# Optimization experiments

Hardware: AMD Instinct MI355X
Metric: run time of the kernel (lower is better)

The kernel has to match this reference:

```python
import jax, jax.numpy as jnp
import numpy as np

HIDDEN = 64
EPS = 0.001


def _gru_cell(x, h, w_ih, w_hh, b_ih, b_hh):
    # PyTorch GRUCell math. w_ih: [3H, D], w_hh: [3H, H], gates ordered (r, z, n).
    gi = x @ w_ih.T + b_ih  # [B, 3H]
    gh = h @ w_hh.T + b_hh  # [B, 3H]
    i_r, i_z, i_n = jnp.split(gi, 3, axis=-1)
    h_r, h_z, h_n = jnp.split(gh, 3, axis=-1)
    r = jax.nn.sigmoid(i_r + h_r)
    z = jax.nn.sigmoid(i_z + h_z)
    n = jnp.tanh(i_n + r * h_n)
    return (1.0 - z) * n + z * h


def setup_inputs() -> dict:
    key = jax.random.key(0)
    ks = jax.random.split(key, 12)
    B, T, state_dim, action_dim = 2048, 512, 64, 8
    H = HIDDEN
    k_in = 1.0 / np.sqrt(H)  # PyTorch GRUCell init bound
    u = lambda k, shp: jax.random.uniform(k, shp, jnp.float32, -k_in, k_in)
    return {
        "state": jax.random.normal(ks[0], (B, T, state_dim), jnp.float32),
        "w_ih1": u(ks[1], (3 * H, state_dim)),
        "w_hh1": u(ks[2], (3 * H, H)),
        "b_ih1": u(ks[3], (3 * H,)),
        "b_hh1": u(ks[4], (3 * H,)),
        "w_ih2": u(ks[5], (3 * H, H)),
        "w_hh2": u(ks[6], (3 * H, H)),
        "b_ih2": u(ks[7], (3 * H,)),
        "b_hh2": u(ks[8], (3 * H,)),
        "fc_w": jax.random.uniform(ks[9], (action_dim, H), jnp.float32, -EPS, EPS),
        "fc_b": u(ks[10], (action_dim,)),
    }


def reference(state, w_ih1, w_hh1, b_ih1, b_hh1, w_ih2, w_hh2, b_ih2, b_hh2, fc_w, fc_b):
    B = state.shape[0]
    h0 = jnp.zeros((B, HIDDEN), state.dtype)

    def step(carry, x_t):
        s1, s2 = carry
        s1 = _gru_cell(x_t, s1, w_ih1, w_hh1, b_ih1, b_hh1)
        s2 = _gru_cell(s1, s2, w_ih2, w_hh2, b_ih2, b_hh2)
        return (s1, s2), None

    xs = jnp.swapaxes(state, 0, 1)  # [T, B, state_dim]
    (_, s2), _ = jax.lax.scan(step, (h0, h0), xs)
    return s2 @ fc_w.T + fc_b  # [B, action_dim]
```

## Files before the change

### kernel.cpp

```cpp
#include <hip/hip_runtime.h>

#define T_STEPS 512
#define HID 64
#define SPB 8
#define NT 512

typedef _Float16 f16x8 __attribute__((ext_vector_type(8)));
typedef float f32x4 __attribute__((ext_vector_type(4)));

#define MFMA(a, b, c) __builtin_amdgcn_mfma_f32_16x16x32_f16(a, b, c, 0, 0, 0)

#define LOG2E 1.44269504088896340736f

__device__ __forceinline__ unsigned pkh(float a, float b) {
    unsigned short ua = __builtin_bit_cast(unsigned short, (_Float16)a);
    unsigned short ub = __builtin_bit_cast(unsigned short, (_Float16)b);
    return (unsigned)ua | ((unsigned)ub << 16);
}
__device__ __forceinline__ float dpp_ror8(float x) {
    int i = __builtin_bit_cast(int, x);
    int r = __builtin_amdgcn_mov_dpp(i, 0x128, 0xF, 0xF, true);
    return __builtin_bit_cast(float, r);
}
__device__ __forceinline__ char* swz(const void* base, int s, int kbyte) {
    int off = s * 128 + kbyte;
    off ^= (s & 7) << 4;
    return (char*)base + off;
}
__device__ __forceinline__ f16x8 g8rowS(const float* __restrict__ p, float s) {
    f16x8 r;
#pragma unroll
    for (int j = 0; j < 8; ++j) r[j] = (_Float16)(p[j] * s);
    return r;
}

#define BAR() do { asm volatile("s_waitcnt lgkmcnt(0)" ::: "memory"); \
                   __builtin_amdgcn_s_barrier();                      \
                   asm volatile("" ::: "memory"); } while (0)

__global__ __launch_bounds__(NT, 1)
void gru2_h16(const float* __restrict__ state,
              const float* __restrict__ w_ih1, const float* __restrict__ w_hh1,
              const float* __restrict__ b_ih1, const float* __restrict__ b_hh1,
              const float* __restrict__ w_ih2, const float* __restrict__ w_hh2,
              const float* __restrict__ b_ih2, const float* __restrict__ b_hh2,
              const float* __restrict__ fc_w,  const float* __restrict__ fc_b,
              float* __restrict__ out)
{
    __shared__ __align__(16) unsigned short xb[2][16][64];
    __shared__ __align__(16) unsigned short h1b[2][16][64];
    __shared__ __align__(16) unsigned short h2b[2][16][64];

    const int tid  = threadIdx.x;
    const int wv8  = tid >> 6;
    const bool isA = wv8 < 4;
    const int w    = wv8 & 3;
    const int lane = tid & 63;
    const int i16  = lane & 15;
    const int g    = lane >> 4;
    const int g8   = g * 8;
    const int b0   = blockIdx.x * SPB;
    const bool realc = (i16 < 8);

    const float* Wp = isA ? w_ih1 : w_ih2;
    const float* Wq = isA ? w_hh1 : w_hh2;
    const float* Bi = isA ? b_ih1 : b_ih2;
    const float* Bh = isA ? b_hh1 : b_hh2;

    const int rA = (16 * w + i16) * HID;
    const int zA = rA + 64 * HID;
    const int nA = rA + 128 * HID;
    f16x8 ar[4], az[4], ani[2], anh[2];
    ar[0]  = g8rowS(Wp + rA + g8, -LOG2E);  ar[1]  = g8rowS(Wp + rA + 32 + g8, -LOG2E);
    ar[2]  = g8rowS(Wq + rA + g8, -LOG2E);  ar[3]  = g8rowS(Wq + rA + 32 + g8, -LOG2E);
    az[0]  = g8rowS(Wp + zA + g8, -LOG2E);  az[1]  = g8rowS(Wp + zA + 32 + g8, -LOG2E);
    az[2]  = g8rowS(Wq + zA + g8, -LOG2E);  az[3]  = g8rowS(Wq + zA + 32 + g8, -LOG2E);
    ani[0] = g8rowS(Wp + nA + g8, 2.0f * LOG2E);
    ani[1] = g8rowS(Wp + nA + 32 + g8, 2.0f * LOG2E);
    anh[0] = g8rowS(Wq + nA + g8, 2.0f * LOG2E);
    anh[1] = g8rowS(Wq + nA + 32 + g8, 2.0f * LOG2E);

    f32x4 bR4, bZ4, bNi4, bNh4;
#pragma unroll
    for (int q = 0; q < 4; ++q) {
        const int r0 = 16 * w + 4 * g + q;
        bR4[q]  = -LOG2E * (Bi[r0] + Bh[r0]);
        bZ4[q]  = -LOG2E * (Bi[64 + r0] + Bh[64 + r0]);
        bNi4[q] = 2.0f * LOG2E * Bi[128 + r0];
        bNh4[q] = 2.0f * LOG2E * Bh[128 + r0];
    }

    char* rp[2][2]; char* rq[2][2]; char* wd[2]; char* sa[2];
    const int scol = i16 & 7;
    const int qb4  = realc ? 0 : 4;
#pragma unroll
    for (int c = 0; c < 2; ++c) {
        const void* Pb = isA ? (const void*)xb[c]      : (const void*)h1b[c ^ 1];
        const void* Qb = isA ? (const void*)h1b[c ^ 1] : (const void*)h2b[c];
        void* Db       = isA ? (void*)h1b[c]           : (void*)h2b[c ^ 1];
        rp[c][0] = swz(Pb, i16, 16 * g);
        rp[c][1] = swz(Pb, i16, 64 + 16 * g);
        rq[c][0] = swz(Qb, i16, 16 * g);
        rq[c][1] = swz(Qb, i16, 64 + 16 * g);
        wd[c]    = swz(Db, scol, 32 * w + 8 * g + qb4);
        sa[c]    = swz(xb[c ^ 1], (tid >> 5) & 7, (tid & 31) * 4);
    }

    for (int k = tid; k < 2 * 16 * 64; k += NT) {
        ((unsigned short*)xb)[k]  = 0;
        ((unsigned short*)h1b)[k] = 0;
        ((unsigned short*)h2b)[k] = 0;
    }
    __syncthreads();

    const int ss = (tid >> 5) & 7;
    const int sk = (tid & 31) * 2;
    const float* xgp = state + (size_t)(b0 + ss) * T_STEPS * HID + sk;
    float2 PF = make_float2(0.0f, 0.0f);
    if (tid < 256) {
        float2 v0 = *(const float2*)xgp;
        *(unsigned*)swz(xb[0], ss, sk * 2) = pkh(v0.x, v0.y);
        PF = *(const float2*)(xgp + HID);
    }
    const float* xnext = xgp + 2 * HID;
    __syncthreads();

    float hr0 = 0.0f, hr1 = 0.0f;
    f16x8 p0 = {}, p1 = {}, q0 = {}, q1 = {};

#define ITER(TT, CUR)                                                            \
  {                                                                              \
    const bool active = isA ? ((TT) < T_STEPS) : ((TT) >= 1);                    \
    if (active) {                                                                \
      if (realc) {       \
        p0 = *(const f16x8*)rp[CUR][0];                                          \
        p1 = *(const f16x8*)rp[CUR][1];                                          \
        q0 = *(const f16x8*)rq[CUR][0];                                          \
        q1 = *(const f16x8*)rq[CUR][1];                                          \
      }                                                                          \
      __builtin_amdgcn_s_setprio(1);                                             \
      f32x4 aR  = MFMA(ar[0], p0, bR4);                                          \
      f32x4 aZ  = MFMA(az[0], p0, bZ4);                                          \
      f32x4 aNi = MFMA(ani[0], p0, bNi4);                                        \
      f32x4 aNh = MFMA(anh[0], q0, bNh4);                                        \
      aR  = MFMA(ar[1], p1, aR);   aR  = MFMA(ar[2], q0, aR);                    \
      aR  = MFMA(ar[3], q1, aR);                                                 \
      aZ  = MFMA(az[1], p1, aZ);   aZ  = MFMA(az[2], q0, aZ);                    \
      aZ  = MFMA(az[3], q1, aZ);                                                 \
      aNi = MFMA(ani[1], p1, aNi);                                               \
      aNh = MFMA(anh[1], q1, aNh);                                               \
      __builtin_amdgcn_s_setprio(0);                                             \
        \
      float vR0  = realc ? aR[0]  : dpp_ror8(aR[2]);                             \
      float vR1  = realc ? aR[1]  : dpp_ror8(aR[3]);                             \
      float vZ0  = realc ? aZ[0]  : dpp_ror8(aZ[2]);                             \
      float vZ1  = realc ? aZ[1]  : dpp_ror8(aZ[3]);                             \
      float vNi0 = realc ? aNi[0] : dpp_ror8(aNi[2]);                            \
      float vNi1 = realc ? aNi[1] : dpp_ror8(aNi[3]);                            \
      float vNh0 = realc ? aNh[0] : dpp_ror8(aNh[2]);                            \
      float vNh1 = realc ? aNh[1] : dpp_ror8(aNh[3]);                            \
      {                                                                          \
        float rg0 = __builtin_amdgcn_rcpf(1.0f + __builtin_amdgcn_exp2f(vR0));   \
        float zg0 = __builtin_amdgcn_rcpf(1.0f + __builtin_amdgcn_exp2f(vZ0));   \
        float e20 = __builtin_amdgcn_exp2f(fmaf(rg0, vNh0, vNi0));               \
        float ng0 = fmaf(-2.0f, __builtin_amdgcn_rcpf(1.0f + e20), 1.0f);        \
        hr0 = fmaf(zg0, hr0 - ng0, ng0);                                         \
        float rg1 = __builtin_amdgcn_rcpf(1.0f + __builtin_amdgcn_exp2f(vR1));   \
        float zg1 = __builtin_amdgcn_rcpf(1.0f + __builtin_amdgcn_exp2f(vZ1));   \
        float e21 = __builtin_amdgcn_exp2f(fmaf(rg1, vNh1, vNi1));               \
        float ng1 = fmaf(-2.0f, __builtin_amdgcn_rcpf(1.0f + e21), 1.0f);        \
        hr1 = fmaf(zg1, hr1 - ng1, ng1);                                         \
      }                                                                          \
      *(unsigned*)wd[CUR] = pkh(hr0, hr1);                                       \
    }                                                                            \
    if (tid < 256 && (TT) < T_STEPS) {                                           \
      *(unsigned*)sa[CUR] = pkh(PF.x, PF.y);                                     \
      PF = *(const float2*)xnext;                                                \
      xnext += ((TT) <= T_STEPS - 4) ? HID : 0;                                  \
    }                                                                            \
    BAR();                                                                       \
  }

    for (int t = 0; t < T_STEPS; t += 2) {
        ITER(t, 0)
        ITER(t + 1, 1)
    }
    ITER(T_STEPS, 0)
#undef ITER

    if (tid < 64) {
        const int s = tid >> 3, a = tid & 7;
        float acc = fc_b[a];
#pragma unroll
        for (int j = 0; j < HID; ++j) {
            _Float16 hv = *(_Float16*)swz(h2b[1], s, j * 2);
            acc = fmaf((float)hv, fc_w[a * HID + j], acc);
        }
        out[(size_t)(b0 + s) * 8 + a] = acc;
    }
}

extern "C" void kernel_launch(void* const* d_in, const int* in_sizes, int n_in,
                              void* d_out, int out_size, void* d_ws, size_t ws_size,
                              hipStream_t stream) {
    (void)in_sizes; (void)n_in; (void)d_ws; (void)ws_size; (void)out_size;
    const float* state = (const float*)d_in[0];
    const float* w_ih1 = (const float*)d_in[1];
    const float* w_hh1 = (const float*)d_in[2];
    const float* b_ih1 = (const float*)d_in[3];
    const float* b_hh1 = (const float*)d_in[4];
    const float* w_ih2 = (const float*)d_in[5];
    const float* w_hh2 = (const float*)d_in[6];
    const float* b_ih2 = (const float*)d_in[7];
    const float* b_hh2 = (const float*)d_in[8];
    const float* fc_w  = (const float*)d_in[9];
    const float* fc_b  = (const float*)d_in[10];
    float* out = (float*)d_out;

    dim3 grid(2048 / SPB);
    dim3 block(NT);
    gru2_h16<<<grid, block, 0, stream>>>(state,
                                         w_ih1, w_hh1, b_ih1, b_hh1,
                                         w_ih2, w_hh2, b_ih2, b_hh2,
                                         fc_w, fc_b, out);
}
```

Before: 237.2 us.

## Load layer-1 input directly into MFMA B-operand registers, drop LDS staging

Each layer-1 wave now prefetches its own slice of the state input from global memory one step ahead into float4 registers. It converts them to f16 MFMA operands in registers instead of staging x through a shared-memory double buffer. This removes the per-step LDS write of x by a separate set of threads and the LDS reads of x by layer-1 waves, which shortens the critical path between barriers. In exchange, each of the four layer-1 waves issues redundant global loads of the same x rows and holds more registers, and global latency must still be hidden within one step.

```diff
diff --git a/kernel.cpp b/kernel.cpp
--- a/kernel.cpp
+++ b/kernel.cpp
@@ -17,6 +17,12 @@
     unsigned short ub = __builtin_bit_cast(unsigned short, (_Float16)b);
     return (unsigned)ua | ((unsigned)ub << 16);
 }
+__device__ __forceinline__ f16x8 cvt8(float4 a, float4 b) {
+    f16x8 r;
+    r[0] = (_Float16)a.x; r[1] = (_Float16)a.y; r[2] = (_Float16)a.z; r[3] = (_Float16)a.w;
+    r[4] = (_Float16)b.x; r[5] = (_Float16)b.y; r[6] = (_Float16)b.z; r[7] = (_Float16)b.w;
+    return r;
+}
 __device__ __forceinline__ float dpp_ror8(float x) {
     int i = __builtin_bit_cast(int, x);
     int r = __builtin_amdgcn_mov_dpp(i, 0x128, 0xF, 0xF, true);
@@ -39,15 +45,14 @@
                    asm volatile("" ::: "memory"); } while (0)
 
 __global__ __launch_bounds__(NT, 1)
-void gru2_h16(const float* __restrict__ state,
-              const float* __restrict__ w_ih1, const float* __restrict__ w_hh1,
-              const float* __restrict__ b_ih1, const float* __restrict__ b_hh1,
-              const float* __restrict__ w_ih2, const float* __restrict__ w_hh2,
-              const float* __restrict__ b_ih2, const float* __restrict__ b_hh2,
-              const float* __restrict__ fc_w,  const float* __restrict__ fc_b,
-              float* __restrict__ out)
+void gru2_xreg(const float* __restrict__ state,
+               const float* __restrict__ w_ih1, const float* __restrict__ w_hh1,
+               const float* __restrict__ b_ih1, const float* __restrict__ b_hh1,
+               const float* __restrict__ w_ih2, const float* __restrict__ w_hh2,
+               const float* __restrict__ b_ih2, const float* __restrict__ b_hh2,
+               const float* __restrict__ fc_w,  const float* __restrict__ fc_b,
+               float* __restrict__ out)
 {
-    __shared__ __align__(16) unsigned short xb[2][16][64];
     __shared__ __align__(16) unsigned short h1b[2][16][64];
     __shared__ __align__(16) unsigned short h2b[2][16][64];
 
@@ -66,6 +71,27 @@
     const float* Wq = isA ? w_hh1 : w_hh2;
     const float* Bi = isA ? b_ih1 : b_ih2;
     const float* Bh = isA ? b_hh1 : b_hh2;
+
+    const float* xl = nullptr;
+    float4 ra0 = {0,0,0,0}, ra1 = {0,0,0,0}, ra2 = {0,0,0,0}, ra3 = {0,0,0,0};
+    f16x8 px0 = {}, px1 = {};
+    if (isA) {
+        const float* xbase = state + (size_t)(b0 + (i16 & 7)) * T_STEPS * HID + g8;
+        if (realc) {
+            ra0 = *(const float4*)(xbase);
+            ra1 = *(const float4*)(xbase + 4);
+            ra2 = *(const float4*)(xbase + 32);
+            ra3 = *(const float4*)(xbase + 36);
+        }
+        px0 = cvt8(ra0, ra1);  px1 = cvt8(ra2, ra3);
+        if (realc) {
+            ra0 = *(const float4*)(xbase + HID);
+            ra1 = *(const float4*)(xbase + HID + 4);
+            ra2 = *(const float4*)(xbase + HID + 32);
+            ra3 = *(const float4*)(xbase + HID + 36);
+        }
+        xl = xbase + 2 * HID;
+    }
 
     const int rA = (16 * w + i16) * HID;
     const int zA = rA + 64 * HID;
@@ -90,12 +116,12 @@
         bNh4[q] = 2.0f * LOG2E * Bh[128 + r0];
     }
 
-    char* rp[2][2]; char* rq[2][2]; char* wd[2]; char* sa[2];
+    char* rp[2][2]; char* rq[2][2]; char* wd[2];
     const int scol = i16 & 7;
     const int qb4  = realc ? 0 : 4;
 #pragma unroll
     for (int c = 0; c < 2; ++c) {
-        const void* Pb = isA ? (const void*)xb[c]      : (const void*)h1b[c ^ 1];
+        const void* Pb = isA ? (const void*)h1b[c]     : (const void*)h1b[c ^ 1];
         const void* Qb = isA ? (const void*)h1b[c ^ 1] : (const void*)h2b[c];
         void* Db       = isA ? (void*)h1b[c]           : (void*)h2b[c ^ 1];
         rp[c][0] = swz(Pb, i16, 16 * g);
@@ -103,26 +129,12 @@
         rq[c][0] = swz(Qb, i16, 16 * g);
         rq[c][1] = swz(Qb, i16, 64 + 16 * g);
         wd[c]    = swz(Db, scol, 32 * w + 8 * g + qb4);
-        sa[c]    = swz(xb[c ^ 1], (tid >> 5) & 7, (tid & 31) * 4);
     }
 
     for (int k = tid; k < 2 * 16 * 64; k += NT) {
-        ((unsigned short*)xb)[k]  = 0;
         ((unsigned short*)h1b)[k] = 0;
         ((unsigned short*)h2b)[k] = 0;
     }
-    __syncthreads();
-
-    const int ss = (tid >> 5) & 7;
-    const int sk = (tid & 31) * 2;
-    const float* xgp = state + (size_t)(b0 + ss) * T_STEPS * HID + sk;
-    float2 PF = make_float2(0.0f, 0.0f);
-    if (tid < 256) {
-        float2 v0 = *(const float2*)xgp;
-        *(unsigned*)swz(xb[0], ss, sk * 2) = pkh(v0.x, v0.y);
-        PF = *(const float2*)(xgp + HID);
-    }
-    const float* xnext = xgp + 2 * HID;
     __syncthreads();
 
     float hr0 = 0.0f, hr1 = 0.0f;
@@ -132,7 +144,13 @@
   {                                                                              \
     const bool active = isA ? ((TT) < T_STEPS) : ((TT) >= 1);                    \
     if (active) {                                                                \
-      if (realc) {       \
+      if (isA) {                                                                 \
+        p0 = px0;  p1 = px1;                   \
+        if (realc) {                                                             \
+          q0 = *(const f16x8*)rq[CUR][0];                                        \
+          q1 = *(const f16x8*)rq[CUR][1];                                        \
+        }                                                                        \
+      } else if (realc) {                                                        \
         p0 = *(const f16x8*)rp[CUR][0];                                          \
         p1 = *(const f16x8*)rp[CUR][1];                                          \
         q0 = *(const f16x8*)rq[CUR][0];                                          \
@@ -150,6 +168,17 @@
       aNi = MFMA(ani[1], p1, aNi);                                               \
       aNh = MFMA(anh[1], q1, aNh);                                               \
       __builtin_amdgcn_s_setprio(0);                                             \
+      if (isA && (TT) < T_STEPS) {          \
+        f16x8 nx0 = cvt8(ra0, ra1), nx1 = cvt8(ra2, ra3);           \
+        if (realc) {                                                             \
+          ra0 = *(const float4*)(xl);                               \
+          ra1 = *(const float4*)(xl + 4);                                        \
+          ra2 = *(const float4*)(xl + 32);                                       \
+          ra3 = *(const float4*)(xl + 36);                                       \
+        }                                                                        \
+        xl += ((TT) <= T_STEPS - 4) ? HID : 0;                                   \
+        px0 = nx0;  px1 = nx1;                                                   \
+      }                                                                          \
         \
       float vR0  = realc ? aR[0]  : dpp_ror8(aR[2]);                             \
       float vR1  = realc ? aR[1]  : dpp_ror8(aR[3]);                             \
@@ -173,11 +202,6 @@
       }                                                                          \
       *(unsigned*)wd[CUR] = pkh(hr0, hr1);                                       \
     }                                                                            \
-    if (tid < 256 && (TT) < T_STEPS) {                                           \
-      *(unsigned*)sa[CUR] = pkh(PF.x, PF.y);                                     \
-      PF = *(const float2*)xnext;                                                \
-      xnext += ((TT) <= T_STEPS - 4) ? HID : 0;                                  \
-    }                                                                            \
     BAR();                                                                       \
   }
 
@@ -219,8 +243,8 @@
 
     dim3 grid(2048 / SPB);
     dim3 block(NT);
-    gru2_h16<<<grid, block, 0, stream>>>(state,
-                                         w_ih1, w_hh1, b_ih1, b_hh1,
-                                         w_ih2, w_hh2, b_ih2, b_hh2,
-                                         fc_w, fc_b, out);
-}
+    gru2_xreg<<<grid, block, 0, stream>>>(state,
+                                          w_ih1, w_hh1, b_ih1, b_hh1,
+                                          w_ih2, w_hh2, b_ih2, b_hh2,
+                                          fc_w, fc_b, out);
+}
```

Result: slower. 546.0 us (+130.2%).

## Collapse each GRU layer onto a single wavefront holding all gate row-blocks

Applied to the files above, without the earlier changes.

Shrinks the block from eight wavefronts to two. Each wavefront now computes all four 16-row blocks of one GRU layer in registers instead of splitting them across four waves. This keeps the per-step barrier at two waves and gives the MFMA unit longer independent chains per wave. In exchange, register pressure rises to about 48 weight fragments per lane, each wave runs four times the serial MFMA and transcendental work per step, and the h2 buffer indexing is reworked to match.

```diff
diff --git a/kernel.cpp b/kernel.cpp
--- a/kernel.cpp
+++ b/kernel.cpp
@@ -2,8 +2,7 @@
 
 #define T_STEPS 512
 #define HID 64
-#define SPB 8
-#define NT 512
+#define NT 128
 
 typedef _Float16 f16x8 __attribute__((ext_vector_type(8)));
 typedef float f32x4 __attribute__((ext_vector_type(4)));
@@ -39,72 +38,80 @@
                    asm volatile("" ::: "memory"); } while (0)
 
 __global__ __launch_bounds__(NT, 1)
-void gru2_h16(const float* __restrict__ state,
-              const float* __restrict__ w_ih1, const float* __restrict__ w_hh1,
-              const float* __restrict__ b_ih1, const float* __restrict__ b_hh1,
-              const float* __restrict__ w_ih2, const float* __restrict__ w_hh2,
-              const float* __restrict__ b_ih2, const float* __restrict__ b_hh2,
-              const float* __restrict__ fc_w,  const float* __restrict__ fc_b,
-              float* __restrict__ out)
+void gru2_rc(const float* __restrict__ state,
+             const float* __restrict__ w_ih1, const float* __restrict__ w_hh1,
+             const float* __restrict__ b_ih1, const float* __restrict__ b_hh1,
+             const float* __restrict__ w_ih2, const float* __restrict__ w_hh2,
+             const float* __restrict__ b_ih2, const float* __restrict__ b_hh2,
+             const float* __restrict__ fc_w,  const float* __restrict__ fc_b,
+             float* __restrict__ out)
 {
     __shared__ __align__(16) unsigned short xb[2][16][64];
     __shared__ __align__(16) unsigned short h1b[2][16][64];
     __shared__ __align__(16) unsigned short h2b[2][16][64];
 
     const int tid  = threadIdx.x;
-    const int wv8  = tid >> 6;
-    const bool isA = wv8 < 4;
-    const int w    = wv8 & 3;
+    const bool isA = (tid < 64);
     const int lane = tid & 63;
     const int i16  = lane & 15;
     const int g    = lane >> 4;
     const int g8   = g * 8;
-    const int b0   = blockIdx.x * SPB;
+    const int b0   = blockIdx.x * 8;
     const bool realc = (i16 < 8);
+    const int scol = i16 & 7;
+    const int qb4  = realc ? 0 : 4;
 
     const float* Wp = isA ? w_ih1 : w_ih2;
     const float* Wq = isA ? w_hh1 : w_hh2;
     const float* Bi = isA ? b_ih1 : b_ih2;
     const float* Bh = isA ? b_hh1 : b_hh2;
 
-    const int rA = (16 * w + i16) * HID;
-    const int zA = rA + 64 * HID;
-    const int nA = rA + 128 * HID;
-    f16x8 ar[4], az[4], ani[2], anh[2];
-    ar[0]  = g8rowS(Wp + rA + g8, -LOG2E);  ar[1]  = g8rowS(Wp + rA + 32 + g8, -LOG2E);
-    ar[2]  = g8rowS(Wq + rA + g8, -LOG2E);  ar[3]  = g8rowS(Wq + rA + 32 + g8, -LOG2E);
-    az[0]  = g8rowS(Wp + zA + g8, -LOG2E);  az[1]  = g8rowS(Wp + zA + 32 + g8, -LOG2E);
-    az[2]  = g8rowS(Wq + zA + g8, -LOG2E);  az[3]  = g8rowS(Wq + zA + 32 + g8, -LOG2E);
-    ani[0] = g8rowS(Wp + nA + g8, 2.0f * LOG2E);
-    ani[1] = g8rowS(Wp + nA + 32 + g8, 2.0f * LOG2E);
-    anh[0] = g8rowS(Wq + nA + g8, 2.0f * LOG2E);
-    anh[1] = g8rowS(Wq + nA + 32 + g8, 2.0f * LOG2E);
-
-    f32x4 bR4, bZ4, bNi4, bNh4;
-#pragma unroll
-    for (int q = 0; q < 4; ++q) {
-        const int r0 = 16 * w + 4 * g + q;
-        bR4[q]  = -LOG2E * (Bi[r0] + Bh[r0]);
-        bZ4[q]  = -LOG2E * (Bi[64 + r0] + Bh[64 + r0]);
-        bNi4[q] = 2.0f * LOG2E * Bi[128 + r0];
-        bNh4[q] = 2.0f * LOG2E * Bh[128 + r0];
-    }
-
-    char* rp[2][2]; char* rq[2][2]; char* wd[2]; char* sa[2];
-    const int scol = i16 & 7;
-    const int qb4  = realc ? 0 : 4;
+    f16x8 wr[4][4], wz[4][4], wni[4][2], wnh[4][2];
+    f32x4 bR[4], bZ[4], bNi[4], bNh[4];
+#pragma unroll
+    for (int rb = 0; rb < 4; ++rb) {
+        const int rA = (rb * 16 + i16) * HID;
+        const int zA = rA + 64 * HID;
+        const int nA = rA + 128 * HID;
+        wr[rb][0]  = g8rowS(Wp + rA + g8, -LOG2E);  wr[rb][1]  = g8rowS(Wp + rA + 32 + g8, -LOG2E);
+        wr[rb][2]  = g8rowS(Wq + rA + g8, -LOG2E);  wr[rb][3]  = g8rowS(Wq + rA + 32 + g8, -LOG2E);
+        wz[rb][0]  = g8rowS(Wp + zA + g8, -LOG2E);  wz[rb][1]  = g8rowS(Wp + zA + 32 + g8, -LOG2E);
+        wz[rb][2]  = g8rowS(Wq + zA + g8, -LOG2E);  wz[rb][3]  = g8rowS(Wq + zA + 32 + g8, -LOG2E);
+        wni[rb][0] = g8rowS(Wp + nA + g8, 2.0f * LOG2E);
+        wni[rb][1] = g8rowS(Wp + nA + 32 + g8, 2.0f * LOG2E);
+        wnh[rb][0] = g8rowS(Wq + nA + g8, 2.0f * LOG2E);
+        wnh[rb][1] = g8rowS(Wq + nA + 32 + g8, 2.0f * LOG2E);
+#pragma unroll
+        for (int q = 0; q < 4; ++q) {
+            const int r0 = rb * 16 + 4 * g + q;
+            bR[rb][q]  = -LOG2E * (Bi[r0] + Bh[r0]);
+            bZ[rb][q]  = -LOG2E * (Bi[64 + r0] + Bh[64 + r0]);
+            bNi[rb][q] = 2.0f * LOG2E * Bi[128 + r0];
+            bNh[rb][q] = 2.0f * LOG2E * Bh[128 + r0];
+        }
+    }
+
+    char* rP[2][2]; char* rQ[2][2]; char* wD[2][4];
 #pragma unroll
     for (int c = 0; c < 2; ++c) {
         const void* Pb = isA ? (const void*)xb[c]      : (const void*)h1b[c ^ 1];
-        const void* Qb = isA ? (const void*)h1b[c ^ 1] : (const void*)h2b[c];
-        void* Db       = isA ? (void*)h1b[c]           : (void*)h2b[c ^ 1];
-        rp[c][0] = swz(Pb, i16, 16 * g);
-        rp[c][1] = swz(Pb, i16, 64 + 16 * g);
-        rq[c][0] = swz(Qb, i16, 16 * g);
-        rq[c][1] = swz(Qb, i16, 64 + 16 * g);
-        wd[c]    = swz(Db, scol, 32 * w + 8 * g + qb4);
-        sa[c]    = swz(xb[c ^ 1], (tid >> 5) & 7, (tid & 31) * 4);
-    }
+        const void* Qb = isA ? (const void*)h1b[c ^ 1] : (const void*)h2b[c ^ 1];
+        void* Db       = isA ? (void*)h1b[c]           : (void*)h2b[c];
+        rP[c][0] = swz(Pb, i16, 16 * g);
+        rP[c][1] = swz(Pb, i16, 64 + 16 * g);
+        rQ[c][0] = swz(Qb, i16, 16 * g);
+        rQ[c][1] = swz(Qb, i16, 64 + 16 * g);
+#pragma unroll
+        for (int rb = 0; rb < 4; ++rb)
+            wD[c][rb] = swz(Db, scol, 32 * rb + 8 * g + qb4);
+    }
+
+    const int sB = lane & 7;
+    const int dB = (lane >> 3) * 8;
+    char* sx[2];
+    sx[0] = swz(xb[1], sB, dB * 2);
+    sx[1] = swz(xb[0], sB, dB * 2);
+    const float* xg = state + (size_t)(b0 + sB) * T_STEPS * HID + dB;
 
     for (int k = tid; k < 2 * 16 * 64; k += NT) {
         ((unsigned short*)xb)[k]  = 0;
@@ -112,88 +119,106 @@
         ((unsigned short*)h2b)[k] = 0;
     }
     __syncthreads();
-
-    const int ss = (tid >> 5) & 7;
-    const int sk = (tid & 31) * 2;
-    const float* xgp = state + (size_t)(b0 + ss) * T_STEPS * HID + sk;
-    float2 PF = make_float2(0.0f, 0.0f);
-    if (tid < 256) {
-        float2 v0 = *(const float2*)xgp;
-        *(unsigned*)swz(xb[0], ss, sk * 2) = pkh(v0.x, v0.y);
-        PF = *(const float2*)(xgp + HID);
-    }
-    const float* xnext = xgp + 2 * HID;
+    float2 PF[4] = {{0,0},{0,0},{0,0},{0,0}};
+    if (!isA) {
+#pragma unroll
+        for (int j = 0; j < 4; ++j) {
+            float2 v = *(const float2*)(xg + 2 * j);
+            *(unsigned*)(sx[1] + 4 * j) = pkh(v.x, v.y);
+        }
+#pragma unroll
+        for (int j = 0; j < 4; ++j) PF[j] = *(const float2*)(xg + HID + 2 * j);
+    }
+    const float* xn = xg + 2 * HID;
     __syncthreads();
 
-    float hr0 = 0.0f, hr1 = 0.0f;
+    float hr[8] = {0, 0, 0, 0, 0, 0, 0, 0};
     f16x8 p0 = {}, p1 = {}, q0 = {}, q1 = {};
-
-#define ITER(TT, CUR)                                                            \
+    f32x4 aR[4], aZ[4], aNi[4], aNh[4];
+
+#define WIN(TT, CUR)                                                             \
   {                                                                              \
     const bool active = isA ? ((TT) < T_STEPS) : ((TT) >= 1);                    \
     if (active) {                                                                \
-      if (realc) {       \
-        p0 = *(const f16x8*)rp[CUR][0];                                          \
-        p1 = *(const f16x8*)rp[CUR][1];                                          \
-        q0 = *(const f16x8*)rq[CUR][0];                                          \
-        q1 = *(const f16x8*)rq[CUR][1];                                          \
+      if (realc) {                                                               \
+        p0 = *(const f16x8*)rP[CUR][0];                                          \
+        p1 = *(const f16x8*)rP[CUR][1];                                          \
+        q0 = *(const f16x8*)rQ[CUR][0];                                          \
+        q1 = *(const f16x8*)rQ[CUR][1];                                          \
       }                                                                          \
       __builtin_amdgcn_s_setprio(1);                                             \
-      f32x4 aR  = MFMA(ar[0], p0, bR4);                                          \
-      f32x4 aZ  = MFMA(az[0], p0, bZ4);                                          \
-      f32x4 aNi = MFMA(ani[0], p0, bNi4);                                        \
-      f32x4 aNh = MFMA(anh[0], q0, bNh4);                                        \
-      aR  = MFMA(ar[1], p1, aR);   aR  = MFMA(ar[2], q0, aR);                    \
-      aR  = MFMA(ar[3], q1, aR);                                                 \
-      aZ  = MFMA(az[1], p1, aZ);   aZ  = MFMA(az[2], q0, aZ);                    \
-      aZ  = MFMA(az[3], q1, aZ);                                                 \
-      aNi = MFMA(ani[1], p1, aNi);                                               \
-      aNh = MFMA(anh[1], q1, aNh);                                               \
+      _Pragma("unroll")                                                          \
+      for (int rb = 0; rb < 4; ++rb) aR[rb]  = MFMA(wr[rb][0], p0, bR[rb]);      \
+      _Pragma("unroll")                                                          \
+      for (int rb = 0; rb < 4; ++rb) aZ[rb]  = MFMA(wz[rb][0], p0, bZ[rb]);      \
+      _Pragma("unroll")                                                          \
+      for (int rb = 0; rb < 4; ++rb) aR[rb]  = MFMA(wr[rb][1], p1, aR[rb]);      \
+      _Pragma("unroll")                                                          \
+      for (int rb = 0; rb < 4; ++rb) aZ[rb]  = MFMA(wz[rb][1], p1, aZ[rb]);      \
+      _Pragma("unroll")                                                          \
+      for (int rb = 0; rb < 4; ++rb) aR[rb]  = MFMA(wr[rb][2], q0, aR[rb]);      \
+      _Pragma("unroll")                                                          \
+      for (int rb = 0; rb < 4; ++rb) aZ[rb]  = MFMA(wz[rb][2], q0, aZ[rb]);      \
+      _Pragma("unroll")                                                          \
+      for (int rb = 0; rb < 4; ++rb) aR[rb]  = MFMA(wr[rb][3], q1, aR[rb]);      \
+      _Pragma("unroll")                                                          \
+      for (int rb = 0; rb < 4; ++rb) aZ[rb]  = MFMA(wz[rb][3], q1, aZ[rb]);      \
+      _Pragma("unroll")                                                          \
+      for (int rb = 0; rb < 4; ++rb) aNi[rb] = MFMA(wni[rb][0], p0, bNi[rb]);    \
+      _Pragma("unroll")                                                          \
+      for (int rb = 0; rb < 4; ++rb) aNi[rb] = MFMA(wni[rb][1], p1, aNi[rb]);    \
+      _Pragma("unroll")                                                          \
+      for (int rb = 0; rb < 4; ++rb) aNh[rb] = MFMA(wnh[rb][0], q0, bNh[rb]);    \
+      _Pragma("unroll")                                                          \
+      for (int rb = 0; rb < 4; ++rb) aNh[rb] = MFMA(wnh[rb][1], q1, aNh[rb]);    \
       __builtin_amdgcn_s_setprio(0);                                             \
-        \
-      float vR0  = realc ? aR[0]  : dpp_ror8(aR[2]);                             \
-      float vR1  = realc ? aR[1]  : dpp_ror8(aR[3]);                             \
-      float vZ0  = realc ? aZ[0]  : dpp_ror8(aZ[2]);                             \
-      float vZ1  = realc ? aZ[1]  : dpp_ror8(aZ[3]);                             \
-      float vNi0 = realc ? aNi[0] : dpp_ror8(aNi[2]);                            \
-      float vNi1 = realc ? aNi[1] : dpp_ror8(aNi[3]);                            \
-      float vNh0 = realc ? aNh[0] : dpp_ror8(aNh[2]);                            \
-      float vNh1 = realc ? aNh[1] : dpp_ror8(aNh[3]);                            \
-      {                                                                          \
+      _Pragma("unroll")                                                          \
+      for (int rb = 0; rb < 4; ++rb) {                                           \
+        float vR0  = realc ? aR[rb][0]  : dpp_ror8(aR[rb][2]);                   \
+        float vR1  = realc ? aR[rb][1]  : dpp_ror8(aR[rb][3]);                   \
+        float vZ0  = realc ? aZ[rb][0]  : dpp_ror8(aZ[rb][2]);                   \
+        float vZ1  = realc ? aZ[rb][1]  : dpp_ror8(aZ[rb][3]);                   \
+        float vNi0 = realc ? aNi[rb][0] : dpp_ror8(aNi[rb][2]);                  \
+        float vNi1 = realc ? aNi[rb][1] : dpp_ror8(aNi[rb][3]);                  \
+        float vNh0 = realc ? aNh[rb][0] : dpp_ror8(aNh[rb][2]);                  \
+        float vNh1 = realc ? aNh[rb][1] : dpp_ror8(aNh[rb][3]);                  \
         float rg0 = __builtin_amdgcn_rcpf(1.0f + __builtin_amdgcn_exp2f(vR0));   \
         float zg0 = __builtin_amdgcn_rcpf(1.0f + __builtin_amdgcn_exp2f(vZ0));   \
         float e20 = __builtin_amdgcn_exp2f(fmaf(rg0, vNh0, vNi0));               \
         float ng0 = fmaf(-2.0f, __builtin_amdgcn_rcpf(1.0f + e20), 1.0f);        \
-        hr0 = fmaf(zg0, hr0 - ng0, ng0);                                         \
+        hr[2 * rb]     = fmaf(zg0, hr[2 * rb] - ng0, ng0);                       \
         float rg1 = __builtin_amdgcn_rcpf(1.0f + __builtin_amdgcn_exp2f(vR1));   \
         float zg1 = __builtin_amdgcn_rcpf(1.0f + __builtin_amdgcn_exp2f(vZ1));   \
         float e21 = __builtin_amdgcn_exp2f(fmaf(rg1, vNh1, vNi1));               \
         float ng1 = fmaf(-2.0f, __builtin_amdgcn_rcpf(1.0f + e21), 1.0f);        \
-        hr1 = fmaf(zg1, hr1 - ng1, ng1);                                         \
+        hr[2 * rb + 1] = fmaf(zg1, hr[2 * rb + 1] - ng1, ng1);                   \
+        *(unsigned*)wD[CUR][rb] = pkh(hr[2 * rb], hr[2 * rb + 1]);               \
       }                                                                          \
-      *(unsigned*)wd[CUR] = pkh(hr0, hr1);                                       \
     }                                                                            \
-    if (tid < 256 && (TT) < T_STEPS) {                                           \
-      *(unsigned*)sa[CUR] = pkh(PF.x, PF.y);                                     \
-      PF = *(const float2*)xnext;                                                \
-      xnext += ((TT) <= T_STEPS - 4) ? HID : 0;                                  \
+    if (!isA && (TT) < T_STEPS) {                                                \
+      _Pragma("unroll")                                                          \
+      for (int j = 0; j < 4; ++j)                                                \
+        *(unsigned*)(sx[CUR] + 4 * j) = pkh(PF[j].x, PF[j].y);      \
+      _Pragma("unroll")                                                          \
+      for (int j = 0; j < 4; ++j) PF[j] = *(const float2*)(xn + 2 * j);          \
+      xn += ((TT) <= T_STEPS - 4) ? HID : 0;                                     \
     }                                                                            \
     BAR();                                                                       \
   }
 
     for (int t = 0; t < T_STEPS; t += 2) {
-        ITER(t, 0)
-        ITER(t + 1, 1)
-    }
-    ITER(T_STEPS, 0)
-#undef ITER
+        WIN(t, 0)
+        WIN(t + 1, 1)
+    }
+    WIN(T_STEPS, 0)
+#undef WIN
 
     if (tid < 64) {
         const int s = tid >> 3, a = tid & 7;
         float acc = fc_b[a];
 #pragma unroll
         for (int j = 0; j < HID; ++j) {
-            _Float16 hv = *(_Float16*)swz(h2b[1], s, j * 2);
+            _Float16 hv = *(_Float16*)swz(h2b[0], s, j * 2);
             acc = fmaf((float)hv, fc_w[a * HID + j], acc);
         }
         out[(size_t)(b0 + s) * 8 + a] = acc;
@@ -217,10 +242,10 @@
     const float* fc_b  = (const float*)d_in[10];
     float* out = (float*)d_out;
 
-    dim3 grid(2048 / SPB);
+    dim3 grid(2048 / 8);
     dim3 block(NT);
-    gru2_h16<<<grid, block, 0, stream>>>(state,
-                                         w_ih1, w_hh1, b_ih1, b_hh1,
-                                         w_ih2, w_hh2, b_ih2, b_hh2,
-                                         fc_w, fc_b, out);
-}
+    gru2_rc<<<grid, block, 0, stream>>>(state,
+                                        w_ih1, w_hh1, b_ih1, b_hh1,
+                                        w_ih2, w_hh2, b_ih2, b_hh2,
+                                        fc_w, fc_b, out);
+}
```

Result: slower. 745.5 us (+214.3%).
